# Optimization experiments

Measured on AMD Instinct MI355X. Metric: run time of the kernel, lower is better.

Reference implementation:

```python
import jax, jax.numpy as jnp
import numpy as np

HASHCODE_LEN = 8   # config.attention_hashcode_len (tau)
NUM_HEAD = 12      # config.num_attention_heads
KERNEL = 9         # config.attention_conv_kernel_size
B, H, S, D = 2, 12, 2048, 64


def _l2_normalize(x, eps=1e-12):
    # yoso.normalize: L2-normalize along last (head_dim) axis
    return x / jnp.maximum(jnp.linalg.norm(x, axis=-1, keepdims=True), eps)


def setup_inputs() -> dict:
    key = jax.random.key(0)
    kq, kk, kv, kw = jax.random.split(key, 4)
    Q = jax.random.normal(kq, (B, H, S, D), jnp.float32)
    K = jax.random.normal(kk, (B, H, S, D), jnp.float32)
    V = jax.random.normal(kv, (B, H, S, D), jnp.float32)
    mask = jnp.ones((B, S), jnp.float32)
    conv_w = jax.random.normal(kw, (H, 1, KERNEL, 1), jnp.float32) * 0.02
    return {"Q": Q, "K": K, "V": V, "mask": mask, "conv_w": conv_w}


def reference(Q, K, V, mask, conv_w):
    # conv skip path: depthwise (groups=num_head) Conv2d over the seq axis of masked V
    Vm = V * mask[:, None, :, None]                       # [B,H,S,D]
    conv_V = jax.lax.conv_general_dilated(
        Vm, conv_w, window_strides=(1, 1),
        padding=((KERNEL // 2, KERNEL // 2), (0, 0)),
        dimension_numbers=("NCHW", "OIHW", "NCHW"),
        feature_group_count=H)

    # yoso_e exact-expectation branch (num_hash_f < 0): normalize Q, K, then
    # attention weight = E[hash collision] = (1 - arccos(q.k)/pi)^hashcode_len
    Qn = _l2_normalize(Q)
    Kn = _l2_normalize(K)
    qk = jnp.einsum("bhsd,bhtd->bhst", Qn, Kn)            # [B,H,S,S]
    qk = jnp.clip(qk, -1.0 + 1e-6, 1.0 - 1e-6)            # keep arccos grad finite
    w = (1.0 - jnp.arccos(qk) / jnp.pi) ** HASHCODE_LEN
    w = w * mask[:, None, None, :]                        # key-side mask
    X = jnp.einsum("bhst,bhtd->bhsd", w, V)
    X = X * mask[:, None, :, None]                        # query-side mask
    X = _l2_normalize(X)                                  # yoso.normalize(X)
    return X + conv_V
```

## Files before the change

kernel.cpp:

```cpp
#include <hip/hip_runtime.h>
#include <hip/hip_bf16.h>
#include <math.h>

typedef __attribute__((ext_vector_type(4)))  float f32x4;
typedef __attribute__((ext_vector_type(16))) float f32x16;
typedef __attribute__((ext_vector_type(8)))  short bf16x8;
typedef __attribute__((ext_vector_type(4)))  int   i32x4;

#define NB 2
#define NH 12
#define NS 2048
#define ND 64
#define NKER 9
#define BH (NB*NH)
#define BHS (NB*NH*NS)
#define NT (NS/64)

using bf16 = __hip_bfloat16;

__device__ __forceinline__ f32x16 mfma32(bf16x8 a, bf16x8 b, f32x16 c) {
  return __builtin_amdgcn_mfma_f32_32x32x16_bf16(a, b, c, 0, 0, 0);
}

__device__ __forceinline__ unsigned short bf16rne(float f) {
  unsigned u = __builtin_bit_cast(unsigned, f);
  u += 0x7FFFu + ((u >> 16) & 1u);
  return (unsigned short)(u >> 16);
}

__global__ __launch_bounds__(256) void prep(
    const float* __restrict__ K, const float* __restrict__ V,
    const float* __restrict__ mask, const float* __restrict__ cw,
    float* __restrict__ out, bf16* __restrict__ Kn, bf16* __restrict__ Vmt) {
  __shared__ float tile[72][68];
  __shared__ float wsm[NKER];
  int bh = blockIdx.y, b = bh / NH, h = bh % NH;
  int s0 = blockIdx.x * 64;
  int tid = threadIdx.x;
  if (tid < NKER) wsm[tid] = cw[h * NKER + tid];

  int r  = tid >> 2;
  int c0 = (tid & 3) * 16;

  {
    const float* Kr = K + ((size_t)bh * NS + s0 + r) * ND + c0;
    float v[16]; float ss = 0.f;
    #pragma unroll
    for (int j = 0; j < 16; ++j) { v[j] = Kr[j]; ss += v[j] * v[j]; }
    ss += __shfl_xor(ss, 1); ss += __shfl_xor(ss, 2);
    float sc = rsqrtf(fmaxf(ss, 1e-24f));
    bf16x8 o0, o1;
    #pragma unroll
    for (int j = 0; j < 8; ++j) {
      o0[j] = (short)bf16rne(v[j] * sc);
      o1[j] = (short)bf16rne(v[8 + j] * sc);
    }
    bf16* dst = Kn + ((size_t)bh * NS + s0 + r) * ND + c0;
    *(bf16x8*)dst = o0; *(bf16x8*)(dst + 8) = o1;
  }

  #pragma unroll
  for (int pass = 0; pass < 2; ++pass) {
    int rr = r + pass * 64;
    if (pass == 0 || tid < 32) {
      int gs = s0 - NKER / 2 + rr;
      bool ok = (gs >= 0 && gs < NS);
      float m = ok ? mask[b * NS + gs] : 0.f;
      #pragma unroll
      for (int j = 0; j < 16; ++j)
        tile[rr][c0 + j] = ok ? V[((size_t)bh * NS + gs) * ND + c0 + j] * m : 0.f;
    }
  }
  __syncthreads();

  {
    float acc[16];
    #pragma unroll
    for (int j = 0; j < 16; ++j) acc[j] = 0.f;
    #pragma unroll
    for (int k = 0; k < NKER; ++k) {
      float w = wsm[k];
      #pragma unroll
      for (int j = 0; j < 16; ++j) acc[j] += tile[r + k][c0 + j] * w;
    }
    float* dst = out + ((size_t)bh * NS + s0 + r) * ND + c0;
    #pragma unroll
    for (int j = 0; j < 16; ++j) dst[j] = acc[j];
  }
  {
    bf16x8 o0, o1;
    #pragma unroll
    for (int j = 0; j < 8; ++j) {
      o0[j] = (short)bf16rne(tile[NKER / 2 + c0 + j][r]);
      o1[j] = (short)bf16rne(tile[NKER / 2 + c0 + 8 + j][r]);
    }
    bf16* dst = Vmt + (size_t)bh * ND * NS + (size_t)r * NS + s0 + c0;
    *(bf16x8*)dst = o0; *(bf16x8*)(dst + 8) = o1;
  }
}

__global__ __launch_bounds__(256) void yoso_attn(
    const float* __restrict__ Q, const bf16* __restrict__ Kn,
    const bf16* __restrict__ Vmt, const float* __restrict__ mask,
    float* __restrict__ out) {
  __shared__ __align__(16) char lds[40 * 1024];

  int tid  = threadIdx.x;
  int wave = tid >> 6;
  int lane = tid & 63;
  int ql   = lane & 31;
  int c    = lane >> 5;
  int qsub = wave >> 1;
  int kh   = wave & 1;
  int bh   = blockIdx.y;
  int b    = bh / NH;
  int q0   = blockIdx.x * 64;

  const bf16* Kbh = Kn  + (size_t)bh * NS * ND;
  const bf16* Vbh = Vmt + (size_t)bh * ND * NS;

  bf16x8 aq[4];
  {
    int qrow = q0 + qsub * 32 + ql;
    const float* Qr = Q + ((size_t)bh * NS + qrow) * ND;
    float qv[32]; float ss = 0.f;
    #pragma unroll
    for (int t = 0; t < 4; ++t) {
      f32x4 a0 = *(const f32x4*)(Qr + t * 16 + c * 8);
      f32x4 a1 = *(const f32x4*)(Qr + t * 16 + c * 8 + 4);
      #pragma unroll
      for (int j = 0; j < 4; ++j) {
        qv[t * 8 + j] = a0[j]; qv[t * 8 + 4 + j] = a1[j];
        ss += a0[j] * a0[j] + a1[j] * a1[j];
      }
    }
    ss += __shfl_xor(ss, 32);
    float sc = rsqrtf(fmaxf(ss, 1e-24f));
    #pragma unroll
    for (int t = 0; t < 4; ++t)
      #pragma unroll
      for (int j = 0; j < 8; ++j)
        aq[t][j] = (short)bf16rne(qv[t * 8 + j] * sc);
  }

  f32x16 xacc[2] = {};

  int srow = tid >> 3;
  int scol = (tid & 7) * 16;
  int sw   = (srow & 7) << 4;
  int d0 = srow * 128 + (scol ^ sw);
  int d1 = (srow + 32) * 128 + (scol ^ sw);
  const char* KsA = (const char*)Kbh + (size_t)srow * 128 + scol;
  const char* KsB = (const char*)Kbh + (size_t)(srow + 32) * 128 + scol;
  const char* VsA = (const char*)Vbh + (size_t)srow * (NS * 2) + scol;
  const char* VsB = (const char*)Vbh + (size_t)(srow + 32) * (NS * 2) + scol;

  *(i32x4*)(lds + d0)        = *(const i32x4*)KsA;
  *(i32x4*)(lds + d1)        = *(const i32x4*)KsB;
  *(i32x4*)(lds + 8192 + d0) = *(const i32x4*)VsA;
  *(i32x4*)(lds + 8192 + d1) = *(const i32x4*)VsB;

  int krow = kh * 32 + ql;
  int ksw  = (krow & 7) << 4;
  int kboff[4];
  #pragma unroll
  for (int t = 0; t < 4; ++t) kboff[t] = krow * 128 + ((t * 32 + c * 16) ^ ksw);
  int pslot_r = ((ql >> 2) & 3) << 4;
  int poff[2];
  #pragma unroll
  for (int ks = 0; ks < 2; ++ks) poff[ks] = ql * 64 + ((ks * 32 + c * 16) ^ pslot_r);
  int bvoff[2][2];
  #pragma unroll
  for (int dt = 0; dt < 2; ++dt) {
    int drow = dt * 32 + ql;
    int vsw  = (drow & 7) << 4;
    #pragma unroll
    for (int ks = 0; ks < 2; ++ks)
      bvoff[dt][ks] = drow * 128 + ((kh * 64 + ks * 32 + c * 16) ^ vsw);
  }

  char* pw = lds + 32768 + wave * 2048;
  i32x4 kA, kB, vA, vB;

  for (int kt = 0; kt < NT; ++kt) {
    __syncthreads();
    if (kt < NT - 1) {
      kA = *(const i32x4*)(KsA + (size_t)(kt + 1) * 8192);
      kB = *(const i32x4*)(KsB + (size_t)(kt + 1) * 8192);
      vA = *(const i32x4*)(VsA + (size_t)(kt + 1) * 128);
      vB = *(const i32x4*)(VsB + (size_t)(kt + 1) * 128);
    }
    char* kb = lds + (kt & 1) * 16384;
    char* vb = kb + 8192;

    f32x16 s{};
    #pragma unroll
    for (int t = 0; t < 4; ++t) {
      bf16x8 bk = *(const bf16x8*)(kb + kboff[t]);
      s = mfma32(aq[t], bk, s);
    }

    #pragma unroll
    for (int r = 0; r < 16; ++r) {
      float x  = s[r];
      float a  = fminf(fabsf(x), 0.999999f);
      float sq = __builtin_amdgcn_sqrtf(1.0f - a);
      float p  = fmaf(fmaf(fmaf(-0.005961377f, a, 0.02363857f), a,
                           -0.06751758f), a, 0.49998939f);
      float u  = sq * p;
      float t1 = (x >= 0.0f) ? (1.0f - u) : u;
      float t2 = t1 * t1, t4 = t2 * t2, w = t4 * t4;
      int q_loc = (r & 3) + 8 * (r >> 2) + 4 * c;
      *(short*)(pw + q_loc * 64 + ((ql * 2) ^ ((((q_loc >> 2) & 3)) << 4))) =
          (short)bf16rne(w);
    }

    #pragma unroll
    for (int ks = 0; ks < 2; ++ks) {
      bf16x8 ap = *(const bf16x8*)(pw + poff[ks]);
      #pragma unroll
      for (int dt = 0; dt < 2; ++dt) {
        bf16x8 bv = *(const bf16x8*)(vb + bvoff[dt][ks]);
        xacc[dt] = mfma32(ap, bv, xacc[dt]);
      }
    }

    if (kt < NT - 1) {
      char* nb = lds + ((kt + 1) & 1) * 16384;
      *(i32x4*)(nb + d0)        = kA;
      *(i32x4*)(nb + d1)        = kB;
      *(i32x4*)(nb + 8192 + d0) = vA;
      *(i32x4*)(nb + 8192 + d1) = vB;
    }
  }

  float* cmb = (float*)lds;
  if (kh == 1) {
    #pragma unroll
    for (int dt = 0; dt < 2; ++dt)
      #pragma unroll
      for (int r = 0; r < 16; ++r) {
        int q_loc = (r & 3) + 8 * (r >> 2) + 4 * c;
        cmb[qsub * 2048 + q_loc * 64 + dt * 32 + ql] = xacc[dt][r];
      }
  }
  __syncthreads();
  if (kh == 0) {
    #pragma unroll
    for (int r = 0; r < 16; ++r) {
      int q_loc = (r & 3) + 8 * (r >> 2) + 4 * c;
      int row = q0 + qsub * 32 + q_loc;
      float m = mask[b * NS + row];
      float x0 = (xacc[0][r] + cmb[qsub * 2048 + q_loc * 64 + ql]) * m;
      float x1 = (xacc[1][r] + cmb[qsub * 2048 + q_loc * 64 + 32 + ql]) * m;
      float s2 = x0 * x0 + x1 * x1;
      #pragma unroll
      for (int mm = 1; mm < 32; mm <<= 1) s2 += __shfl_xor(s2, mm);
      float sc = rsqrtf(fmaxf(s2, 1e-24f));
      size_t base = ((size_t)bh * NS + row) * ND;
      out[base + ql]      += x0 * sc;
      out[base + 32 + ql] += x1 * sc;
    }
  }
}

extern "C" void kernel_launch(void* const* d_in, const int* in_sizes, int n_in,
                              void* d_out, int out_size, void* d_ws, size_t ws_size,
                              hipStream_t stream) {
  const float* Q    = (const float*)d_in[0];
  const float* K    = (const float*)d_in[1];
  const float* V    = (const float*)d_in[2];
  const float* mask = (const float*)d_in[3];
  const float* cw   = (const float*)d_in[4];
  float* out = (float*)d_out;

  bf16* Kn  = (bf16*)d_ws;
  bf16* Vmt = Kn + (size_t)BHS * ND;

  prep<<<dim3(NS / 64, BH), 256, 0, stream>>>(K, V, mask, cw, out, Kn, Vmt);
  yoso_attn<<<dim3(NS / 64, BH), 256, 0, stream>>>(Q, Kn, Vmt, mask, out);
}
```

Before: 89.54 us.

## Drop LDS staging; split keys across four waves with direct global loads

```diff
diff --git a/kernel.cpp b/kernel.cpp
--- a/kernel.cpp
+++ b/kernel.cpp
@@ -14,7 +14,6 @@
 #define NKER 9
 #define BH (NB*NH)
 #define BHS (NB*NH*NS)
-#define NT (NS/64)
 
 using bf16 = __hip_bfloat16;
 
@@ -26,6 +25,12 @@
   unsigned u = __builtin_bit_cast(unsigned, f);
   u += 0x7FFFu + ((u >> 16) & 1u);
   return (unsigned short)(u >> 16);
+}
+
+__device__ __forceinline__ int cvtpk_bf16(float lo, float hi) {
+  int d;
+  asm("v_cvt_pk_bf16_f32 %0, %1, %2" : "=v"(d) : "v"(lo), "v"(hi));
+  return d;
 }
 
 __global__ __launch_bounds__(256) void prep(
@@ -103,25 +108,26 @@
     const float* __restrict__ Q, const bf16* __restrict__ Kn,
     const bf16* __restrict__ Vmt, const float* __restrict__ mask,
     float* __restrict__ out) {
-  __shared__ __align__(16) char lds[40 * 1024];
+  __shared__ float cmb[3][32][64];
 
   int tid  = threadIdx.x;
-  int wave = tid >> 6;
+  int kh   = tid >> 6;
   int lane = tid & 63;
   int ql   = lane & 31;
   int c    = lane >> 5;
-  int qsub = wave >> 1;
-  int kh   = wave & 1;
-  int bh   = blockIdx.y;
-  int b    = bh / NH;
-  int q0   = blockIdx.x * 64;
+
+  int bx = blockIdx.x;
+  int bh = ((bx >> 3) / 64) * 8 + (bx & 7);
+  int qg = (bx >> 3) & 63;
+  int b  = bh / NH;
+  int q0 = qg * 32;
 
   const bf16* Kbh = Kn  + (size_t)bh * NS * ND;
   const bf16* Vbh = Vmt + (size_t)bh * ND * NS;
 
   bf16x8 aq[4];
   {
-    int qrow = q0 + qsub * 32 + ql;
+    int qrow = q0 + ql;
     const float* Qr = Q + ((size_t)bh * NS + qrow) * ND;
     float qv[32]; float ss = 0.f;
     #pragma unroll
@@ -143,116 +149,84 @@
         aq[t][j] = (short)bf16rne(qv[t * 8 + j] * sc);
   }
 
-  f32x16 xacc[2] = {};
-
-  int srow = tid >> 3;
-  int scol = (tid & 7) * 16;
-  int sw   = (srow & 7) << 4;
-  int d0 = srow * 128 + (scol ^ sw);
-  int d1 = (srow + 32) * 128 + (scol ^ sw);
-  const char* KsA = (const char*)Kbh + (size_t)srow * 128 + scol;
-  const char* KsB = (const char*)Kbh + (size_t)(srow + 32) * 128 + scol;
-  const char* VsA = (const char*)Vbh + (size_t)srow * (NS * 2) + scol;
-  const char* VsB = (const char*)Vbh + (size_t)(srow + 32) * (NS * 2) + scol;
-
-  *(i32x4*)(lds + d0)        = *(const i32x4*)KsA;
-  *(i32x4*)(lds + d1)        = *(const i32x4*)KsB;
-  *(i32x4*)(lds + 8192 + d0) = *(const i32x4*)VsA;
-  *(i32x4*)(lds + 8192 + d1) = *(const i32x4*)VsB;
-
-  int krow = kh * 32 + ql;
-  int ksw  = (krow & 7) << 4;
-  int kboff[4];
-  #pragma unroll
-  for (int t = 0; t < 4; ++t) kboff[t] = krow * 128 + ((t * 32 + c * 16) ^ ksw);
-  int pslot_r = ((ql >> 2) & 3) << 4;
-  int poff[2];
-  #pragma unroll
-  for (int ks = 0; ks < 2; ++ks) poff[ks] = ql * 64 + ((ks * 32 + c * 16) ^ pslot_r);
-  int bvoff[2][2];
-  #pragma unroll
-  for (int dt = 0; dt < 2; ++dt) {
-    int drow = dt * 32 + ql;
-    int vsw  = (drow & 7) << 4;
-    #pragma unroll
-    for (int ks = 0; ks < 2; ++ks)
-      bvoff[dt][ks] = drow * 128 + ((kh * 64 + ks * 32 + c * 16) ^ vsw);
-  }
-
-  char* pw = lds + 32768 + wave * 2048;
-  i32x4 kA, kB, vA, vB;
-
-  for (int kt = 0; kt < NT; ++kt) {
-    __syncthreads();
-    if (kt < NT - 1) {
-      kA = *(const i32x4*)(KsA + (size_t)(kt + 1) * 8192);
-      kB = *(const i32x4*)(KsB + (size_t)(kt + 1) * 8192);
-      vA = *(const i32x4*)(VsA + (size_t)(kt + 1) * 128);
-      vB = *(const i32x4*)(VsB + (size_t)(kt + 1) * 128);
-    }
-    char* kb = lds + (kt & 1) * 16384;
-    char* vb = kb + 8192;
+  f32x16 xa0{}, xa1{};
+
+  const char* kp  = (const char*)Kbh + (size_t)(kh * 512 + ql) * 128 + c * 16;
+  const char* vp0 = (const char*)Vbh + (size_t)ql * (NS * 2) + kh * 1024 + c * 16;
+  const char* vp1 = vp0 + (size_t)32 * (NS * 2);
+
+  #pragma unroll 1
+  for (int kt = 0; kt < 16; ++kt) {
+    const char* kpt  = kp + (size_t)kt * (32 * 128);
+    const char* vpt0 = vp0 + kt * 64;
+    const char* vpt1 = vp1 + kt * 64;
+    bf16x8 ak0 = *(const bf16x8*)(kpt);
+    bf16x8 ak1 = *(const bf16x8*)(kpt + 32);
+    bf16x8 ak2 = *(const bf16x8*)(kpt + 64);
+    bf16x8 ak3 = *(const bf16x8*)(kpt + 96);
+    bf16x8 bv00 = *(const bf16x8*)(vpt0);
+    bf16x8 bv01 = *(const bf16x8*)(vpt0 + 32);
+    bf16x8 bv10 = *(const bf16x8*)(vpt1);
+    bf16x8 bv11 = *(const bf16x8*)(vpt1 + 32);
 
     f32x16 s{};
-    #pragma unroll
-    for (int t = 0; t < 4; ++t) {
-      bf16x8 bk = *(const bf16x8*)(kb + kboff[t]);
-      s = mfma32(aq[t], bk, s);
-    }
-
+    s = mfma32(ak0, aq[0], s);
+    s = mfma32(ak1, aq[1], s);
+    s = mfma32(ak2, aq[2], s);
+    s = mfma32(ak3, aq[3], s);
+
+    int pk[8];
+    #pragma unroll
+    for (int g = 0; g < 4; ++g) {
+      float wq[4];
+      #pragma unroll
+      for (int j = 0; j < 4; ++j) {
+        float x = s[g * 4 + j];
+        float a = fminf(fabsf(x), 0.999999f);
+        float sq = __builtin_amdgcn_sqrtf(1.0f - a);
+        float p = fmaf(fmaf(fmaf(-0.005961377f, a, 0.02363857f), a,
+                            -0.06751758f), a, 0.49998939f);
+        float u = sq * p;
+        float t1 = (x >= 0.0f) ? (1.0f - u) : u;
+        float t2 = t1 * t1, t4 = t2 * t2;
+        wq[j] = t4 * t4;
+      }
+      pk[g * 2]     = cvtpk_bf16(wq[0], wq[1]);
+      pk[g * 2 + 1] = cvtpk_bf16(wq[2], wq[3]);
+    }
+    int xpk[8];
+    #pragma unroll
+    for (int i = 0; i < 8; ++i) xpk[i] = __shfl_xor(pk[i], 32);
+    i32x4 pa0i = c ? (i32x4){xpk[2], xpk[3], pk[2], pk[3]}
+                   : (i32x4){pk[0], pk[1], xpk[0], xpk[1]};
+    i32x4 pa1i = c ? (i32x4){xpk[6], xpk[7], pk[6], pk[7]}
+                   : (i32x4){pk[4], pk[5], xpk[4], xpk[5]};
+    bf16x8 pa0 = __builtin_bit_cast(bf16x8, pa0i);
+    bf16x8 pa1 = __builtin_bit_cast(bf16x8, pa1i);
+
+    xa0 = mfma32(pa0, bv00, xa0);
+    xa1 = mfma32(pa0, bv10, xa1);
+    xa0 = mfma32(pa1, bv01, xa0);
+    xa1 = mfma32(pa1, bv11, xa1);
+  }
+
+  if (kh != 0) {
     #pragma unroll
     for (int r = 0; r < 16; ++r) {
-      float x  = s[r];
-      float a  = fminf(fabsf(x), 0.999999f);
-      float sq = __builtin_amdgcn_sqrtf(1.0f - a);
-      float p  = fmaf(fmaf(fmaf(-0.005961377f, a, 0.02363857f), a,
-                           -0.06751758f), a, 0.49998939f);
-      float u  = sq * p;
-      float t1 = (x >= 0.0f) ? (1.0f - u) : u;
-      float t2 = t1 * t1, t4 = t2 * t2, w = t4 * t4;
-      int q_loc = (r & 3) + 8 * (r >> 2) + 4 * c;
-      *(short*)(pw + q_loc * 64 + ((ql * 2) ^ ((((q_loc >> 2) & 3)) << 4))) =
-          (short)bf16rne(w);
-    }
-
-    #pragma unroll
-    for (int ks = 0; ks < 2; ++ks) {
-      bf16x8 ap = *(const bf16x8*)(pw + poff[ks]);
-      #pragma unroll
-      for (int dt = 0; dt < 2; ++dt) {
-        bf16x8 bv = *(const bf16x8*)(vb + bvoff[dt][ks]);
-        xacc[dt] = mfma32(ap, bv, xacc[dt]);
-      }
-    }
-
-    if (kt < NT - 1) {
-      char* nb = lds + ((kt + 1) & 1) * 16384;
-      *(i32x4*)(nb + d0)        = kA;
-      *(i32x4*)(nb + d1)        = kB;
-      *(i32x4*)(nb + 8192 + d0) = vA;
-      *(i32x4*)(nb + 8192 + d1) = vB;
-    }
-  }
-
-  float* cmb = (float*)lds;
-  if (kh == 1) {
-    #pragma unroll
-    for (int dt = 0; dt < 2; ++dt)
-      #pragma unroll
-      for (int r = 0; r < 16; ++r) {
-        int q_loc = (r & 3) + 8 * (r >> 2) + 4 * c;
-        cmb[qsub * 2048 + q_loc * 64 + dt * 32 + ql] = xacc[dt][r];
-      }
+      int qrow = (r & 3) + 8 * (r >> 2) + 4 * c;
+      cmb[kh - 1][qrow][ql]      = xa0[r];
+      cmb[kh - 1][qrow][32 + ql] = xa1[r];
+    }
   }
   __syncthreads();
   if (kh == 0) {
     #pragma unroll
     for (int r = 0; r < 16; ++r) {
-      int q_loc = (r & 3) + 8 * (r >> 2) + 4 * c;
-      int row = q0 + qsub * 32 + q_loc;
-      float m = mask[b * NS + row];
-      float x0 = (xacc[0][r] + cmb[qsub * 2048 + q_loc * 64 + ql]) * m;
-      float x1 = (xacc[1][r] + cmb[qsub * 2048 + q_loc * 64 + 32 + ql]) * m;
+      int qrow = (r & 3) + 8 * (r >> 2) + 4 * c;
+      int row  = q0 + qrow;
+      float m  = mask[b * NS + row];
+      float x0 = (xa0[r] + cmb[0][qrow][ql] + cmb[1][qrow][ql] + cmb[2][qrow][ql]) * m;
+      float x1 = (xa1[r] + cmb[0][qrow][32 + ql] + cmb[1][qrow][32 + ql] + cmb[2][qrow][32 + ql]) * m;
       float s2 = x0 * x0 + x1 * x1;
       #pragma unroll
       for (int mm = 1; mm < 32; mm <<= 1) s2 += __shfl_xor(s2, mm);
@@ -278,5 +252,5 @@
   bf16* Vmt = Kn + (size_t)BHS * ND;
 
   prep<<<dim3(NS / 64, BH), 256, 0, stream>>>(K, V, mask, cw, out, Kn, Vmt);
-  yoso_attn<<<dim3(NS / 64, BH), 256, 0, stream>>>(Q, Kn, Vmt, mask, out);
-}
+  yoso_attn<<<(NS / 32) * BH, 256, 0, stream>>>(Q, Kn, Vmt, mask, out);
+}
```

New measurement: 117.3 us. +31.0%, slower.
